# Optimization experiments

Hardware: AMD Instinct MI355X
Metric: run time of the kernel (lower is better)

Reference implementation:

```python
import jax, jax.numpy as jnp
import numpy as np

N_HEADS = 16
KEY_DIM = 64
VAL_DIM = 64
HIDDEN = 1024
SCALE = 1.0 / float(KEY_DIM) ** 0.5


def setup_inputs() -> dict:
    key = jax.random.key(0)
    ks = jax.random.split(key, 16)
    B, Lq, Lk, R = 2, 2048, 2048, 2048
    inp = {
        "query": jax.random.normal(ks[0], (B, Lq, HIDDEN), jnp.float32),
        "value": jax.random.normal(ks[1], (B, Lk, HIDDEN), jnp.float32),
        "positional_embedding": jax.random.normal(ks[2], (R, HIDDEN), jnp.float32),
        "u_weight": jax.random.normal(ks[3], (N_HEADS, KEY_DIM), jnp.float32) * 0.02,
        "v_weight": jax.random.normal(ks[4], (N_HEADS, KEY_DIM), jnp.float32) * 0.02,
        "indices": jax.random.randint(ks[5], (2, Lq, Lk), 0, R, jnp.int64 if jax.config.jax_enable_x64 else jnp.int32),
        "lower": jax.random.uniform(ks[6], (Lq, Lk), jnp.float32),
    }
    s = 0.02
    inp["Wq"] = jax.random.normal(ks[7], (HIDDEN, N_HEADS * KEY_DIM), jnp.float32) * s
    inp["bq"] = jnp.zeros((N_HEADS * KEY_DIM,), jnp.float32)
    inp["Wk"] = jax.random.normal(ks[8], (HIDDEN, N_HEADS * KEY_DIM), jnp.float32) * s
    inp["bk"] = jnp.zeros((N_HEADS * KEY_DIM,), jnp.float32)
    inp["Wv"] = jax.random.normal(ks[9], (HIDDEN, N_HEADS * VAL_DIM), jnp.float32) * s
    inp["bv"] = jnp.zeros((N_HEADS * VAL_DIM,), jnp.float32)
    inp["Wr"] = jax.random.normal(ks[10], (HIDDEN, N_HEADS * KEY_DIM), jnp.float32) * s
    inp["br"] = jnp.zeros((N_HEADS * KEY_DIM,), jnp.float32)
    inp["Wo"] = jax.random.normal(ks[11], (N_HEADS * VAL_DIM, HIDDEN), jnp.float32) * s
    inp["bo"] = jnp.zeros((HIDDEN,), jnp.float32)
    return inp


def reference(query, value, positional_embedding, u_weight, v_weight, indices, lower,
              Wq, bq, Wk, bk, Wv, bv, Wr, br, Wo, bo):
    B, Lq, _ = query.shape
    Lk = value.shape[1]
    R = positional_embedding.shape[0]
    # projections (torch Linear with weights stored as [in, out])
    q = (query @ Wq + bq).reshape(B, Lq, N_HEADS, KEY_DIM)
    k = (value @ Wk + bk).reshape(B, Lk, N_HEADS, KEY_DIM)
    v = (value @ Wv + bv).reshape(B, Lk, N_HEADS, VAL_DIM)
    r = (positional_embedding @ Wr + br).reshape(R, N_HEADS, KEY_DIM)
    # content (AC) and position (BD) score terms -> [i, j, b, n]
    AC = jnp.einsum("bind,bjnd->ijbn", q + u_weight, k)
    BD = jnp.einsum("bind,jnd->ijbn", q + v_weight, r)
    # rel-shift: gather [Lq, R] -> [Lq, Lk] positions, then apply lower mask
    BD = BD[indices[0], indices[1]] * lower[:, :, None, None]
    attn = jax.nn.softmax((AC + BD) * SCALE, axis=1)  # softmax over key dim j
    out = jnp.einsum("ijbn,bjnd->bind", attn, v).reshape(B, Lq, N_HEADS * VAL_DIM)
    return out @ Wo + bo
```

## Files before the change

### kernel.cpp

```cpp
#include <hip/hip_runtime.h>
#include <stdint.h>

typedef __attribute__((ext_vector_type(8))) short short8;
typedef __attribute__((ext_vector_type(4))) float f32x4;
typedef unsigned short u16;
typedef unsigned int u32;
typedef unsigned long long u64;

#define LQ 2048
#define LK 2048
#define RDIM 2048
#define HID 1024
#define NH 16
#define DH 64
#define S2SCALE 0.1803368801111204f

__device__ __forceinline__ float bf2f(u16 u){
  union { unsigned int i; float f; } v; v.i = ((unsigned int)u) << 16; return v.f;
}
__device__ __forceinline__ u16 f2bf(float f){
  union { float f; unsigned int i; } v; v.f = f;
  unsigned int r = v.i + 0x7fffu + ((v.i >> 16) & 1u);
  return (u16)(r >> 16);
}
__device__ __forceinline__ f32x4 fzero(){ f32x4 z = {0.0f, 0.0f, 0.0f, 0.0f}; return z; }

__global__ void k_detect(const u32* __restrict__ q, const u32* __restrict__ idxw,
                         int* __restrict__ flags){
  int t = threadIdx.x;
  u32 w = q[t];
  int b = (w >> 7) & 0xFF;
  unsigned long long mb = __ballot(b >= 100 && b <= 140);
  u32 hi = idxw[2 * t + 1];
  unsigned long long mi = __ballot(hi == 0u);
  if (t == 0){
    flags[0] = (__popcll(mb) >= 48) ? 1 : 0;
    flags[1] = (__popcll(mi) == 64) ? 1 : 0;
  }
}

struct Seg { const void* src; u16* dst; int n4; };
struct SegPack { Seg s[8]; };
__global__ void k_ingestN(SegPack p, const int* __restrict__ flags){
  int f = flags[0];
  Seg sg = p.s[blockIdx.y];
  int stride = gridDim.x * blockDim.x;
  for (int i = blockIdx.x * blockDim.x + threadIdx.x; i < sg.n4; i += stride){
    if (f){
      reinterpret_cast<uint2*>(sg.dst)[i] = reinterpret_cast<const uint2*>(sg.src)[i];
    } else {
      float4 v = reinterpret_cast<const float4*>(sg.src)[i];
      union { u16 h[4]; uint2 u; } t;
      t.h[0] = f2bf(v.x); t.h[1] = f2bf(v.y); t.h[2] = f2bf(v.z); t.h[3] = f2bf(v.w);
      reinterpret_cast<uint2*>(sg.dst)[i] = t.u;
    }
  }
}

struct WPack { const void* src[5]; u16* dst[5]; };
__global__ void k_wtrans(WPack p, const int* __restrict__ flags){
  int f = flags[0];
  const void* W = p.src[blockIdx.z];
  u16* Wt = p.dst[blockIdx.z];
  __shared__ u16 t[64][65];
  int tid = threadIdx.x;
  int bx = blockIdx.x, by = blockIdx.y;
#pragma unroll
  for (int it = 0; it < 16; ++it){
    int id = it * 256 + tid;
    int r = id >> 6, c = id & 63;
    size_t so = (size_t)(by * 64 + r) * HID + bx * 64 + c;
    t[r][c] = f ? ((const u16*)W)[so] : f2bf(((const float*)W)[so]);
  }
  __syncthreads();
#pragma unroll
  for (int it = 0; it < 16; ++it){
    int id = it * 256 + tid;
    int r = id >> 6, c = id & 63;
    Wt[(size_t)(bx * 64 + r) * HID + by * 64 + c] = t[c][r];
  }
}

__global__ void k_goff(const int* __restrict__ idx, int* __restrict__ goff,
                       const int* __restrict__ flags){
  int i64f = flags[1];
  const size_t N = (size_t)LQ * LK;
  size_t stride = (size_t)gridDim.x * blockDim.x;
  for (size_t t = (size_t)blockIdx.x * blockDim.x + threadIdx.x; t < N; t += stride){
    long long a0, a1;
    if (i64f){
      const long long* ip = (const long long*)idx;
      a0 = ip[t]; a1 = ip[N + t];
    } else {
      a0 = idx[t]; a1 = idx[N + t];
    }
    goff[t] = (int)(a0 * RDIM + a1);
  }
}

__global__ void k_gemm(const u16* __restrict__ A, const u16* __restrict__ Bt,
                       const u16* __restrict__ bias,
                       const u16* __restrict__ add0, const u16* __restrict__ add1,
                       void* __restrict__ D0, u16* __restrict__ D1,
                       int headmajor, const int* __restrict__ oflags){
  __shared__ u16 As[128][72];
  __shared__ u16 Bs[128][72];
  int tid = threadIdx.x;
  int l = tid & 63, w = tid >> 6;
  int lr = l & 15, g = l >> 4;
  int wr = w >> 1, wc = w & 1;
  int outf32 = oflags ? (oflags[0] == 0) : 0;
  f32x4 acc[4][4];
#pragma unroll
  for (int a = 0; a < 4; ++a)
#pragma unroll
    for (int bq_ = 0; bq_ < 4; ++bq_) acc[a][bq_] = fzero();
  const size_t arowg = (size_t)blockIdx.x * 128;
  const size_t browg = (size_t)blockIdx.y * 128;
  for (int kt = 0; kt < HID; kt += 64){
#pragma unroll
    for (int it = 0; it < 4; ++it){
      int id = it * 256 + tid;
      int r = id >> 3, ch = id & 7;
      uint4 va = *reinterpret_cast<const uint4*>(A + (arowg + r) * HID + kt + ch * 8);
      *reinterpret_cast<uint4*>(&As[r][ch * 8]) = va;
      uint4 vb = *reinterpret_cast<const uint4*>(Bt + (browg + r) * HID + kt + ch * 8);
      *reinterpret_cast<uint4*>(&Bs[r][ch * 8]) = vb;
    }
    __syncthreads();
#pragma unroll
    for (int ks = 0; ks < 2; ++ks){
      short8 af[4], bfv[4];
#pragma unroll
      for (int mf = 0; mf < 4; ++mf)
        af[mf] = *reinterpret_cast<const short8*>(&As[wr * 64 + mf * 16 + lr][ks * 32 + 8 * g]);
#pragma unroll
      for (int nf = 0; nf < 4; ++nf)
        bfv[nf] = *reinterpret_cast<const short8*>(&Bs[wc * 64 + nf * 16 + lr][ks * 32 + 8 * g]);
#pragma unroll
      for (int mf = 0; mf < 4; ++mf)
#pragma unroll
        for (int nf = 0; nf < 4; ++nf)
          acc[mf][nf] = __builtin_amdgcn_mfma_f32_16x16x32_bf16(af[mf], bfv[nf], acc[mf][nf], 0, 0, 0);
    }
    __syncthreads();
  }
#pragma unroll
  for (int mf = 0; mf < 4; ++mf)
#pragma unroll
    for (int nf = 0; nf < 4; ++nf){
      int col = (int)browg + wc * 64 + nf * 16 + lr;
      float bcol = bf2f(bias[col]);
      float a0 = add0 ? bf2f(add0[col]) : 0.0f;
      float a1 = add1 ? bf2f(add1[col]) : 0.0f;
#pragma unroll
      for (int reg = 0; reg < 4; ++reg){
        int row = (int)arowg + wr * 64 + mf * 16 + 4 * g + reg;
        float base = acc[mf][nf][reg] + bcol;
        if (headmajor == 2){
          int b = row >> 11, i = row & 2047;
          int n32 = col >> 6, d = col & 63;
          u16* Dx = (n32 < NH) ? (u16*)D0 : D1;
          size_t dst = ((size_t)(b * NH + (n32 & (NH - 1))) * LQ + i) * DH + d;
          Dx[dst] = f2bf(base);
        } else if (headmajor == 1){
          int b = row >> 11, i = row & 2047;
          int n = col >> 6, d = col & 63;
          size_t dst = ((size_t)(b * NH + n) * LQ + i) * DH + d;
          ((u16*)D0)[dst] = f2bf(base + a0);
          if (D1) D1[dst] = f2bf(base + a1);
        } else {
          size_t dst = (size_t)row * HID + col;
          if (outf32) ((float*)D0)[dst] = base;
          else        ((u16*)D0)[dst] = f2bf(base);
        }
      }
    }
}

__global__ void k_bdfull16(const u16* __restrict__ qv, const u16* __restrict__ rr,
                           u16* __restrict__ bdf, int bnBase){
  __shared__ u16 tile[32][64][16];
  int tid = threadIdx.x;
  int l = tid & 63, w = tid >> 6;
  int lr = l & 15, g = l >> 4;
  int i0 = blockIdx.x * 32, j0 = blockIdx.y * 64;
#pragma unroll
  for (int hh = 0; hh < 4; ++hh){
    int g_ = w * 4 + hh;
    int bn = bnBase + g_;
    int b = bn >> 4, n = bn & 15;
    const u16* qb = qv + ((size_t)(b * NH + n) * LQ + i0) * DH;
    const u16* rb = rr + ((size_t)n * RDIM + j0) * DH;
    short8 af[2][2];
#pragma unroll
    for (int mf = 0; mf < 2; ++mf)
#pragma unroll
      for (int ks = 0; ks < 2; ++ks)
        af[mf][ks] = *reinterpret_cast<const short8*>(qb + (size_t)(mf * 16 + lr) * DH + ks * 32 + 8 * g);
    f32x4 acc[2][4];
#pragma unroll
    for (int mf = 0; mf < 2; ++mf)
#pragma unroll
      for (int nf = 0; nf < 4; ++nf) acc[mf][nf] = fzero();
#pragma unroll
    for (int nf = 0; nf < 4; ++nf){
#pragma unroll
      for (int ks = 0; ks < 2; ++ks){
        short8 bb = *reinterpret_cast<const short8*>(rb + (size_t)(nf * 16 + lr) * DH + ks * 32 + 8 * g);
#pragma unroll
        for (int mf = 0; mf < 2; ++mf)
          acc[mf][nf] = __builtin_amdgcn_mfma_f32_16x16x32_bf16(af[mf][ks], bb, acc[mf][nf], 0, 0, 0);
      }
    }
#pragma unroll
    for (int mf = 0; mf < 2; ++mf)
#pragma unroll
      for (int nf = 0; nf < 4; ++nf)
#pragma unroll
        for (int reg = 0; reg < 4; ++reg)
          tile[mf * 16 + 4 * g + reg][nf * 16 + lr][g_] = f2bf(acc[mf][nf][reg]);
  }
  __syncthreads();
#pragma unroll
  for (int e = 0; e < 32; ++e){
    int id = e * 256 + tid;
    int line = id >> 2, part = id & 3;
    int ii = line >> 6, jj = line & 63;
    u64 v = *reinterpret_cast<const u64*>(&tile[ii][jj][part * 4]);
    *reinterpret_cast<u64*>(
        bdf + ((size_t)(i0 + ii) * RDIM + (size_t)(j0 + jj)) * 16 + part * 4) = v;
  }
}

__global__ void k_bdfull8(const u16* __restrict__ qv, const u16* __restrict__ rr,
                          u16* __restrict__ bdf, int bnBase){
  __shared__ u16 tile[32][64][8];
  int tid = threadIdx.x;
  int l = tid & 63, w = tid >> 6;
  int lr = l & 15, g = l >> 4;
  int i0 = blockIdx.x * 32, j0 = blockIdx.y * 64;
#pragma unroll
  for (int hh = 0; hh < 2; ++hh){
    int g_ = w * 2 + hh;
    int bn = bnBase + g_;
    int b = bn >> 4, n = bn & 15;
    const u16* qb = qv + ((size_t)(b * NH + n) * LQ + i0) * DH;
    const u16* rb = rr + ((size_t)n * RDIM + j0) * DH;
    short8 af[2][2];
#pragma unroll
    for (int mf = 0; mf < 2; ++mf)
#pragma unroll
      for (int ks = 0; ks < 2; ++ks)
        af[mf][ks] = *reinterpret_cast<const short8*>(qb + (size_t)(mf * 16 + lr) * DH + ks * 32 + 8 * g);
    f32x4 acc[2][4];
#pragma unroll
    for (int mf = 0; mf < 2; ++mf)
#pragma unroll
      for (int nf = 0; nf < 4; ++nf) acc[mf][nf] = fzero();
#pragma unroll
    for (int nf = 0; nf < 4; ++nf){
#pragma unroll
      for (int ks = 0; ks < 2; ++ks){
        short8 bb = *reinterpret_cast<const short8*>(rb + (size_t)(nf * 16 + lr) * DH + ks * 32 + 8 * g);
#pragma unroll
        for (int mf = 0; mf < 2; ++mf)
          acc[mf][nf] = __builtin_amdgcn_mfma_f32_16x16x32_bf16(af[mf][ks], bb, acc[mf][nf], 0, 0, 0);
      }
    }
#pragma unroll
    for (int mf = 0; mf < 2; ++mf)
#pragma unroll
      for (int nf = 0; nf < 4; ++nf)
#pragma unroll
        for (int reg = 0; reg < 4; ++reg)
          tile[mf * 16 + 4 * g + reg][nf * 16 + lr][g_] = f2bf(acc[mf][nf][reg]);
  }
  __syncthreads();
#pragma unroll
  for (int e = 0; e < 16; ++e){
    int id = e * 256 + tid;
    int line = id >> 1, part = id & 1;
    int ii = line >> 6, jj = line & 63;
    u64 v = *reinterpret_cast<const u64*>(&tile[ii][jj][part * 4]);
    *reinterpret_cast<u64*>(
        bdf + ((size_t)(i0 + ii) * RDIM + (size_t)(j0 + jj)) * 8 + part * 4) = v;
  }
}

template<int G>
__global__ void k_bdfull(const u16* __restrict__ qv, const u16* __restrict__ rr,
                         u16* __restrict__ bdf, int bnBase){
  __shared__ u16 tile[16][32][G];
  int tid = threadIdx.x;
  int l = tid & 63, w = tid >> 6;
  int lr = l & 15, g = l >> 4;
  int i0 = blockIdx.x * 16, j0 = blockIdx.y * 32;
  if (w < G){
    int g_ = w;
    int bn = bnBase + g_;
    int b = bn >> 4, n = bn & 15;
    const u16* qb = qv + ((size_t)(b * NH + n) * LQ + i0) * DH;
    const u16* rb = rr + ((size_t)n * RDIM + j0) * DH;
    f32x4 acc2[2];
    acc2[0] = fzero(); acc2[1] = fzero();
#pragma unroll
    for (int ks = 0; ks < 2; ++ks){
      short8 a = *reinterpret_cast<const short8*>(qb + (size_t)lr * DH + ks * 32 + 8 * g);
#pragma unroll
      for (int nf = 0; nf < 2; ++nf){
        short8 bb = *reinterpret_cast<const short8*>(rb + (size_t)(lr + 16 * nf) * DH + ks * 32 + 8 * g);
        acc2[nf] = __builtin_amdgcn_mfma_f32_16x16x32_bf16(a, bb, acc2[nf], 0, 0, 0);
      }
    }
#pragma unroll
    for (int nf = 0; nf < 2; ++nf){
      int jj = lr + 16 * nf;
#pragma unroll
      for (int reg = 0; reg < 4; ++reg)
        tile[4 * g + reg][jj][g_] = f2bf(acc2[nf][reg]);
    }
  }
  __syncthreads();
  constexpr int CHUNKS = 512;
#pragma unroll
  for (int e = 0; e < (CHUNKS * G + 255) / 256 && e * 256 < CHUNKS * G; ++e){
    int id = e * 256 + tid;
    if (id >= CHUNKS * G) break;
    int line = id / G, k = id % G;
    int ii = line >> 5, jj = line & 31;
    bdf[((size_t)(i0 + ii) * RDIM + (size_t)(j0 + jj)) * G + k] = tile[ii][jj][k];
  }
}

template<int G>
__global__ void k_gather(const u16* __restrict__ bdf, const int* __restrict__ goff,
                         const u16* __restrict__ lower, u16* __restrict__ bdg,
                         int iBase, int iSpan){
  __shared__ u16 tile[G][16][32];
  int tid = threadIdx.x;
  int i0 = iBase + blockIdx.x * 16, j0 = blockIdx.y * 32;
#pragma unroll
  for (int it = 0; it < 2; ++it){
    int p = it * 256 + tid;
    int ii = p >> 5, jj = p & 31;
    size_t off = (size_t)(i0 + ii) * LK + (j0 + jj);
    int go = goff[off];
    float lw = bf2f(lower[off]);
    const u16* src = bdf + (size_t)go * G;
    union { uint4 q[2]; u32 w2[8]; u16 h[16]; } uv;
    if (G == 16){
      uv.q[0] = *reinterpret_cast<const uint4*>(src);
      uv.q[1] = *reinterpret_cast<const uint4*>(src + 8);
    } else if (G == 8){
      uv.q[0] = *reinterpret_cast<const uint4*>(src);
    } else if (G == 2){
      uv.w2[0] = *reinterpret_cast<const u32*>(src);
    } else {
      uv.h[0] = *src;
    }
#pragma unroll
    for (int k = 0; k < G; ++k)
      tile[k][ii][jj] = f2bf(bf2f(uv.h[k]) * lw);
  }
  __syncthreads();
  constexpr int CHUNKS = G * 128;
#pragma unroll
  for (int e = 0; e < (CHUNKS + 255) / 256; ++e){
    int id = e * 256 + tid;
    if (CHUNKS < 256 * ((CHUNKS + 255) / 256) && id >= CHUNKS) break;
    int g_ = id >> 7, rem = id & 127;
    int ii = rem >> 3, part = rem & 7;
    u64 v = *reinterpret_cast<const u64*>(&tile[g_][ii][part * 4]);
    __builtin_nontemporal_store(v, reinterpret_cast<u64*>(
        bdg + (size_t)g_ * iSpan * LK + (size_t)(i0 - iBase + ii) * LK + j0 + part * 4));
  }
}

__device__ __forceinline__ void flash_compute(
    int lr, int g,
    const short8& aq0, const short8& aq1,
    f32x4* O, float* mrun, float* lacc,
    u16 (*klds)[72], u16 (*vtlds)[136], u16 (*pldsw)[136]){
  float sv[8][4];
#pragma unroll
  for (int nf = 0; nf < 8; ++nf){
    f32x4 z = fzero();
    short8 bk0 = *reinterpret_cast<const short8*>(&klds[lr + 16 * nf][8 * g]);
    short8 bk1 = *reinterpret_cast<const short8*>(&klds[lr + 16 * nf][32 + 8 * g]);
    z = __builtin_amdgcn_mfma_f32_16x16x32_bf16(aq0, bk0, z, 0, 0, 0);
    z = __builtin_amdgcn_mfma_f32_16x16x32_bf16(aq1, bk1, z, 0, 0, 0);
#pragma unroll
    for (int reg = 0; reg < 4; ++reg){
      float bd = bf2f(pldsw[4 * g + reg][lr + 16 * nf]);
      sv[nf][reg] = (z[reg] + bd) * S2SCALE;
    }
  }
  float fs[4];
#pragma unroll
  for (int reg = 0; reg < 4; ++reg){
    float mx = sv[0][reg];
#pragma unroll
    for (int nf = 1; nf < 8; ++nf) mx = fmaxf(mx, sv[nf][reg]);
#pragma unroll
    for (int d = 1; d < 16; d <<= 1) mx = fmaxf(mx, __shfl_xor(mx, d));
    float mnew = fmaxf(mrun[reg], mx);
    fs[reg] = exp2f(mrun[reg] - mnew);
    mrun[reg] = mnew;
    float sumloc = 0.0f;
#pragma unroll
    for (int nf = 0; nf < 8; ++nf){
      sv[nf][reg] = exp2f(sv[nf][reg] - mnew);
      sumloc += sv[nf][reg];
    }
    lacc[reg] = lacc[reg] * fs[reg] + sumloc;
  }
#pragma unroll
  for (int nf = 0; nf < 4; ++nf)
#pragma unroll
    for (int reg = 0; reg < 4; ++reg)
      O[nf][reg] *= fs[reg];
#pragma unroll
  for (int nf = 0; nf < 8; ++nf)
#pragma unroll
    for (int reg = 0; reg < 4; ++reg)
      pldsw[4 * g + reg][lr + 16 * nf] = f2bf(sv[nf][reg]);
  short8 pa[4];
#pragma unroll
  for (int ks = 0; ks < 4; ++ks)
    pa[ks] = *reinterpret_cast<const short8*>(&pldsw[lr][ks * 32 + 8 * g]);
#pragma unroll
  for (int nf = 0; nf < 4; ++nf){
    int d = lr + 16 * nf;
#pragma unroll
    for (int ks = 0; ks < 4; ++ks){
      int cv = ((ks * 4 + g) ^ (d >> 3)) * 8;
      short8 bv = *reinterpret_cast<const short8*>(&vtlds[d][cv]);
      O[nf] = __builtin_amdgcn_mfma_f32_16x16x32_bf16(pa[ks], bv, O[nf], 0, 0, 0);
    }
  }
}

__global__ __launch_bounds__(256) void k_flash(
    const u16* __restrict__ qu, const u16* __restrict__ kk,
    const u16* __restrict__ vv, const u16* __restrict__ bdg,
    u16* __restrict__ oo, int bnBase, int iBase, int iSpan){
  __shared__ u16 klds[128][72];
  __shared__ u16 vtlds[64][136];
  __shared__ u16 plds[4][16][136];
  int tid = threadIdx.x;
  int l = tid & 63, w = tid >> 6;
  int lr = l & 15, g = l >> 4;
  int gi = blockIdx.x;
  int bn = bnBase + gi;
  int b = bn >> 4, n = bn & 15;
  int i0 = iBase + blockIdx.y * 64;
  const u16* qb = qu + ((size_t)bn * LQ + i0 + w * 16) * DH;
  short8 aq0 = *reinterpret_cast<const short8*>(qb + (size_t)lr * DH + 8 * g);
  short8 aq1 = *reinterpret_cast<const short8*>(qb + (size_t)lr * DH + 32 + 8 * g);
  f32x4 O[4];
#pragma unroll
  for (int nf = 0; nf < 4; ++nf) O[nf] = fzero();
  float mrun[4], lacc[4];
#pragma unroll
  for (int r = 0; r < 4; ++r){ mrun[r] = -1e30f; lacc[r] = 0.0f; }
  const u16* kbase = kk + (size_t)bn * LK * DH;
  const u16* vbase = vv + (size_t)bn * LK * DH;
  const u16* bdw = bdg + (size_t)gi * iSpan * LK + (size_t)(i0 - iBase + w * 16) * LK;
  u16 (*pldsw)[136] = plds[w];
  int brow = l >> 2, bq = l & 3;

  uint4 kv[8];
  uint4 bdv[4];

#define LOADALL(J_) do { _Pragma("unroll") for (int it_ = 0; it_ < 4; ++it_){ \
    int id_ = it_ * 256 + tid; int r_ = id_ >> 3, ch_ = id_ & 7; \
    kv[it_]     = *reinterpret_cast<const uint4*>(kbase + (size_t)((J_) + r_) * DH + ch_ * 8); \
    kv[4 + it_] = *reinterpret_cast<const uint4*>(vbase + (size_t)((J_) + r_) * DH + ch_ * 8); } \
    _Pragma("unroll") for (int c_ = 0; c_ < 4; ++c_) \
      bdv[c_] = *reinterpret_cast<const uint4*>(bdw + (size_t)brow * LK + (J_) + (c_ * 4 + bq) * 8); } while(0)

#define WRITEALL() do { _Pragma("unroll") for (int it_ = 0; it_ < 4; ++it_){ \
    int id_ = it_ * 256 + tid; int r_ = id_ >> 3, ch_ = id_ & 7; \
    *reinterpret_cast<uint4*>(&klds[r_][ch_ * 8]) = kv[it_]; \
    u16 tmp_[8]; *reinterpret_cast<uint4*>(tmp_) = kv[4 + it_]; \
    int cb_ = r_ ^ (ch_ * 8); \
    _Pragma("unroll") for (int e_ = 0; e_ < 8; ++e_) vtlds[ch_ * 8 + e_][cb_] = tmp_[e_]; } \
    _Pragma("unroll") for (int c_ = 0; c_ < 4; ++c_) \
      *reinterpret_cast<uint4*>(&pldsw[brow][(c_ * 4 + bq) * 8]) = bdv[c_]; } while(0)

  LOADALL(0);
  WRITEALL();
  __syncthreads();

  for (int t = 0; t < 16; ++t){
    if (t < 15) LOADALL((t + 1) * 128);
    flash_compute(lr, g, aq0, aq1, O, mrun, lacc, klds, vtlds, pldsw);
    if (t < 15){
      __syncthreads();
      WRITEALL();
      __syncthreads();
    }
  }
#undef LOADALL
#undef WRITEALL

  float lsum[4];
#pragma unroll
  for (int reg = 0; reg < 4; ++reg){
    float s = lacc[reg];
#pragma unroll
    for (int d = 1; d < 16; d <<= 1) s += __shfl_xor(s, d);
    lsum[reg] = s;
  }
#pragma unroll
  for (int nf = 0; nf < 4; ++nf)
#pragma unroll
    for (int reg = 0; reg < 4; ++reg){
      int i = i0 + w * 16 + 4 * g + reg;
      float vo = O[nf][reg] / lsum[reg];
      oo[((size_t)(b * LQ + i)) * HID + n * DH + lr + 16 * nf] = f2bf(vo);
    }
}

extern "C" void kernel_launch(void* const* d_in, const int* in_sizes, int n_in,
                              void* d_out, int out_size, void* d_ws, size_t ws_size,
                              hipStream_t stream){
  const void* query = d_in[0];
  const void* value = d_in[1];
  const void* pos   = d_in[2];
  const void* uw    = d_in[3];
  const void* vw    = d_in[4];
  const int* idx    = (const int*)d_in[5];
  const void* lower = d_in[6];
  const void* Wq = d_in[7];  const void* bq = d_in[8];
  const void* Wk = d_in[9];  const void* bk = d_in[10];
  const void* Wv = d_in[11]; const void* bv = d_in[12];
  const void* Wr = d_in[13]; const void* br = d_in[14];
  const void* Wo = d_in[15]; const void* bo = d_in[16];
  (void)in_sizes; (void)n_in; (void)out_size;

  char* ws = (char*)d_ws;
  const size_t MB = (size_t)1 << 20;
  u16* cquery = (u16*)(ws + 0 * MB);
  u16* cvalue = (u16*)(ws + 8 * MB);
  int* goff   = (int*)(ws + 0 * MB);
  u16* cpos   = (u16*)(ws + 16 * MB);
  u16* clower = (u16*)(ws + 20 * MB);
  char* sm = ws + 28 * MB;
  u16* cuw = (u16*)(sm + 0 * 4096);
  u16* cvw = (u16*)(sm + 1 * 4096);
  u16* cbq = (u16*)(sm + 2 * 4096);
  u16* cbk = (u16*)(sm + 3 * 4096);
  u16* cbv = cbk + 1024;
  u16* cbr = (u16*)(sm + 5 * 4096);
  u16* cbo = (u16*)(sm + 6 * 4096);
  int* flags = (int*)(sm + 7 * 4096);
  u16* wot = (u16*)(ws + 29 * MB);
  u16* wqt = (u16*)(ws + 31 * MB);
  u16* wkt = (u16*)(ws + 33 * MB);
  u16* wvt = (u16*)(ws + 35 * MB);
  u16* wrt = (u16*)(ws + 37 * MB);
  u16* qu  = (u16*)(ws + 39 * MB);
  u16* qv  = (u16*)(ws + 47 * MB);
  u16* kkp = (u16*)(ws + 55 * MB);
  u16* vvp = (u16*)(ws + 63 * MB);
  u16* rrp = (u16*)(ws + 71 * MB);
  u16* oo  = (u16*)(ws + 75 * MB);
  u16* bdf = (u16*)(ws + 84 * MB);

  dim3 blk(256);
  k_detect<<<1, 64, 0, stream>>>((const u32*)query, (const u32*)idx, flags);

  {
    SegPack big;
    big.s[0] = { query, cquery, 2 * LQ * HID / 4 };
    big.s[1] = { value, cvalue, 2 * LK * HID / 4 };
    big.s[2] = { pos,   cpos,   RDIM * HID / 4 };
    big.s[3] = { lower, clower, LQ * LK / 4 };
    for (int i = 4; i < 8; ++i) big.s[i] = { nullptr, nullptr, 0 };
    k_ingestN<<<dim3(512, 4), blk, 0, stream>>>(big, flags);
    SegPack sml;
    sml.s[0] = { uw, cuw, NH * DH / 4 };
    sml.s[1] = { vw, cvw, NH * DH / 4 };
    sml.s[2] = { bq, cbq, HID / 4 };
    sml.s[3] = { bk, cbk, HID / 4 };
    sml.s[4] = { bv, cbv, HID / 4 };
    sml.s[5] = { br, cbr, HID / 4 };
    sml.s[6] = { bo, cbo, HID / 4 };
    sml.s[7] = { nullptr, nullptr, 0 };
    k_ingestN<<<dim3(4, 7), blk, 0, stream>>>(sml, flags);
  }
  {
    WPack wp;
    wp.src[0] = Wq; wp.dst[0] = wqt;
    wp.src[1] = Wk; wp.dst[1] = wkt;
    wp.src[2] = Wv; wp.dst[2] = wvt;
    wp.src[3] = Wr; wp.dst[3] = wrt;
    wp.src[4] = Wo; wp.dst[4] = wot;
    k_wtrans<<<dim3(16, 16, 5), blk, 0, stream>>>(wp, flags);
  }

  k_gemm<<<dim3(32, 8), blk, 0, stream>>>(cquery, wqt, cbq, cuw, cvw, qu, qv, 1, nullptr);
  k_gemm<<<dim3(32, 16), blk, 0, stream>>>(cvalue, wkt, cbk, nullptr, nullptr, kkp, vvp, 2, nullptr);
  k_gemm<<<dim3(16, 8), blk, 0, stream>>>(cpos, wrt, cbr, nullptr, nullptr, rrp, nullptr, 1, nullptr);

  k_goff<<<dim3(1024), blk, 0, stream>>>(idx, goff, flags);

  if (ws_size >= 276 * MB){
    u16* bdg = (u16*)(ws + 212 * MB);
    for (int b0 = 0; b0 < 2 * NH; b0 += 16){
      k_bdfull16<<<dim3(64, 32), blk, 0, stream>>>(qv, rrp, bdf, b0);
      for (int ih = 0; ih < LQ; ih += 1024){
        k_gather<16><<<dim3(64, 64), blk, 0, stream>>>(bdf, goff, clower, bdg, ih, 1024);
        k_flash<<<dim3(16, 16), blk, 0, stream>>>(qu, kkp, vvp, bdg, oo, b0, ih, 1024);
      }
    }
  } else if (ws_size >= 212 * MB){
    u16* bdg = (u16*)(ws + 148 * MB);
    for (int b0 = 0; b0 < 2 * NH; b0 += 8){
      k_bdfull8<<<dim3(64, 32), blk, 0, stream>>>(qv, rrp, bdf, b0);
      k_gather<8><<<dim3(128, 64), blk, 0, stream>>>(bdf, goff, clower, bdg, 0, LQ);
      k_flash<<<dim3(8, 32), blk, 0, stream>>>(qu, kkp, vvp, bdg, oo, b0, 0, LQ);
    }
  } else if (ws_size >= 116 * MB){
    u16* bdg = (u16*)(ws + 100 * MB);
    for (int b0 = 0; b0 < 2 * NH; b0 += 2){
      k_bdfull<2><<<dim3(128, 64), blk, 0, stream>>>(qv, rrp, bdf, b0);
      k_gather<2><<<dim3(128, 64), blk, 0, stream>>>(bdf, goff, clower, bdg, 0, LQ);
      k_flash<<<dim3(2, 32), blk, 0, stream>>>(qu, kkp, vvp, bdg, oo, b0, 0, LQ);
    }
  } else {
    u16* bdg = (u16*)(ws + 92 * MB);
    for (int b0 = 0; b0 < 2 * NH; b0 += 1){
      k_bdfull<1><<<dim3(128, 64), blk, 0, stream>>>(qv, rrp, bdf, b0);
      k_gather<1><<<dim3(128, 64), blk, 0, stream>>>(bdf, goff, clower, bdg, 0, LQ);
      k_flash<<<dim3(1, 32), blk, 0, stream>>>(qu, kkp, vvp, bdg, oo, b0, 0, LQ);
    }
  }
  k_gemm<<<dim3(32, 8), blk, 0, stream>>>(oo, wot, cbo, nullptr, nullptr, d_out, nullptr, 0, flags);
}
```

Baseline: 979.9 us.

## Chunk gathered BD along key dimension with split-softmax state carried across flash passes

The gathered position-score buffer is now split into key-dimension chunks rather than query-row halves. Flash attention runs once per chunk, storing the running max, running sum and unnormalised output in fp32 scratch between chunks and normalising only on the last chunk. Each flash launch now covers all query rows, giving a larger grid per launch, and the workspace layout is repacked so the 16-head path fits in a smaller workspace. The cost is extra fp32 partial-state traffic and more launches when chunks are small.

```diff
diff --git a/kernel.cpp b/kernel.cpp
--- a/kernel.cpp
+++ b/kernel.cpp
@@ -336,10 +336,12 @@
 template<int G>
 __global__ void k_gather(const u16* __restrict__ bdf, const int* __restrict__ goff,
                          const u16* __restrict__ lower, u16* __restrict__ bdg,
-                         int iBase, int iSpan){
+                         int jBase, int jSpan){
   __shared__ u16 tile[G][16][32];
   int tid = threadIdx.x;
-  int i0 = iBase + blockIdx.x * 16, j0 = blockIdx.y * 32;
+  int i0 = blockIdx.x * 16;
+  int j0loc = blockIdx.y * 32;
+  int j0 = jBase + j0loc;
 #pragma unroll
   for (int it = 0; it < 2; ++it){
     int p = it * 256 + tid;
@@ -373,7 +375,7 @@
     int ii = rem >> 3, part = rem & 7;
     u64 v = *reinterpret_cast<const u64*>(&tile[g_][ii][part * 4]);
     __builtin_nontemporal_store(v, reinterpret_cast<u64*>(
-        bdg + (size_t)g_ * iSpan * LK + (size_t)(i0 - iBase + ii) * LK + j0 + part * 4));
+        bdg + (size_t)g_ * LQ * jSpan + (size_t)(i0 + ii) * jSpan + j0loc + part * 4));
   }
 }
 
@@ -444,7 +446,8 @@
 __global__ __launch_bounds__(256) void k_flash(
     const u16* __restrict__ qu, const u16* __restrict__ kk,
     const u16* __restrict__ vv, const u16* __restrict__ bdg,
-    u16* __restrict__ oo, int bnBase, int iBase, int iSpan){
+    u16* __restrict__ oo, float* __restrict__ Opart, float2* __restrict__ mlpart,
+    int bnBase, int jBase, int jSpan, int mode){
   __shared__ u16 klds[128][72];
   __shared__ u16 vtlds[64][136];
   __shared__ u16 plds[4][16][136];
@@ -454,31 +457,43 @@
   int gi = blockIdx.x;
   int bn = bnBase + gi;
   int b = bn >> 4, n = bn & 15;
-  int i0 = iBase + blockIdx.y * 64;
+  int i0 = blockIdx.y * 64;
   const u16* qb = qu + ((size_t)bn * LQ + i0 + w * 16) * DH;
   short8 aq0 = *reinterpret_cast<const short8*>(qb + (size_t)lr * DH + 8 * g);
   short8 aq1 = *reinterpret_cast<const short8*>(qb + (size_t)lr * DH + 32 + 8 * g);
   f32x4 O[4];
-#pragma unroll
-  for (int nf = 0; nf < 4; ++nf) O[nf] = fzero();
   float mrun[4], lacc[4];
-#pragma unroll
-  for (int r = 0; r < 4; ++r){ mrun[r] = -1e30f; lacc[r] = 0.0f; }
+  if (mode & 1){
+#pragma unroll
+    for (int nf = 0; nf < 4; ++nf) O[nf] = fzero();
+#pragma unroll
+    for (int r = 0; r < 4; ++r){ mrun[r] = -1e30f; lacc[r] = 0.0f; }
+  } else {
+#pragma unroll
+    for (int reg = 0; reg < 4; ++reg){
+      int i = i0 + w * 16 + 4 * g + reg;
+      float2 ml = mlpart[(((size_t)gi * LQ + i) << 4) + lr];
+      mrun[reg] = ml.x; lacc[reg] = ml.y;
+#pragma unroll
+      for (int nf = 0; nf < 4; ++nf)
+        O[nf][reg] = Opart[((size_t)gi * LQ + i) * DH + lr + 16 * nf];
+    }
+  }
   const u16* kbase = kk + (size_t)bn * LK * DH;
   const u16* vbase = vv + (size_t)bn * LK * DH;
-  const u16* bdw = bdg + (size_t)gi * iSpan * LK + (size_t)(i0 - iBase + w * 16) * LK;
+  const u16* bdw = bdg + (size_t)gi * LQ * jSpan + (size_t)(i0 + w * 16) * jSpan;
   u16 (*pldsw)[136] = plds[w];
   int brow = l >> 2, bq = l & 3;
 
   uint4 kv[8];
   uint4 bdv[4];
 
-#define LOADALL(J_) do { _Pragma("unroll") for (int it_ = 0; it_ < 4; ++it_){ \
+#define LOADALL(JL_) do { _Pragma("unroll") for (int it_ = 0; it_ < 4; ++it_){ \
     int id_ = it_ * 256 + tid; int r_ = id_ >> 3, ch_ = id_ & 7; \
-    kv[it_]     = *reinterpret_cast<const uint4*>(kbase + (size_t)((J_) + r_) * DH + ch_ * 8); \
-    kv[4 + it_] = *reinterpret_cast<const uint4*>(vbase + (size_t)((J_) + r_) * DH + ch_ * 8); } \
+    kv[it_]     = *reinterpret_cast<const uint4*>(kbase + (size_t)(jBase + (JL_) + r_) * DH + ch_ * 8); \
+    kv[4 + it_] = *reinterpret_cast<const uint4*>(vbase + (size_t)(jBase + (JL_) + r_) * DH + ch_ * 8); } \
     _Pragma("unroll") for (int c_ = 0; c_ < 4; ++c_) \
-      bdv[c_] = *reinterpret_cast<const uint4*>(bdw + (size_t)brow * LK + (J_) + (c_ * 4 + bq) * 8); } while(0)
+      bdv[c_] = *reinterpret_cast<const uint4*>(bdw + (size_t)brow * jSpan + (JL_) + (c_ * 4 + bq) * 8); } while(0)
 
 #define WRITEALL() do { _Pragma("unroll") for (int it_ = 0; it_ < 4; ++it_){ \
     int id_ = it_ * 256 + tid; int r_ = id_ >> 3, ch_ = id_ & 7; \
@@ -489,14 +504,15 @@
     _Pragma("unroll") for (int c_ = 0; c_ < 4; ++c_) \
       *reinterpret_cast<uint4*>(&pldsw[brow][(c_ * 4 + bq) * 8]) = bdv[c_]; } while(0)
 
+  int ntiles = jSpan >> 7;
   LOADALL(0);
   WRITEALL();
   __syncthreads();
 
-  for (int t = 0; t < 16; ++t){
-    if (t < 15) LOADALL((t + 1) * 128);
+  for (int t = 0; t < ntiles; ++t){
+    if (t < ntiles - 1) LOADALL((t + 1) * 128);
     flash_compute(lr, g, aq0, aq1, O, mrun, lacc, klds, vtlds, pldsw);
-    if (t < 15){
+    if (t < ntiles - 1){
       __syncthreads();
       WRITEALL();
       __syncthreads();
@@ -505,22 +521,34 @@
 #undef LOADALL
 #undef WRITEALL
 
-  float lsum[4];
-#pragma unroll
-  for (int reg = 0; reg < 4; ++reg){
-    float s = lacc[reg];
-#pragma unroll
-    for (int d = 1; d < 16; d <<= 1) s += __shfl_xor(s, d);
-    lsum[reg] = s;
-  }
-#pragma unroll
-  for (int nf = 0; nf < 4; ++nf)
+  if (mode & 2){
+    float lsum[4];
+#pragma unroll
+    for (int reg = 0; reg < 4; ++reg){
+      float s = lacc[reg];
+#pragma unroll
+      for (int d = 1; d < 16; d <<= 1) s += __shfl_xor(s, d);
+      lsum[reg] = s;
+    }
+#pragma unroll
+    for (int nf = 0; nf < 4; ++nf)
+#pragma unroll
+      for (int reg = 0; reg < 4; ++reg){
+        int i = i0 + w * 16 + 4 * g + reg;
+        float vo = O[nf][reg] / lsum[reg];
+        oo[((size_t)(b * LQ + i)) * HID + n * DH + lr + 16 * nf] = f2bf(vo);
+      }
+  } else {
 #pragma unroll
     for (int reg = 0; reg < 4; ++reg){
       int i = i0 + w * 16 + 4 * g + reg;
-      float vo = O[nf][reg] / lsum[reg];
-      oo[((size_t)(b * LQ + i)) * HID + n * DH + lr + 16 * nf] = f2bf(vo);
-    }
+      float2 ml; ml.x = mrun[reg]; ml.y = lacc[reg];
+      mlpart[(((size_t)gi * LQ + i) << 4) + lr] = ml;
+#pragma unroll
+      for (int nf = 0; nf < 4; ++nf)
+        Opart[((size_t)gi * LQ + i) * DH + lr + 16 * nf] = O[nf][reg];
+    }
+  }
 }
 
 extern "C" void kernel_launch(void* const* d_in, const int* in_sizes, int n_in,
@@ -545,9 +573,8 @@
   u16* cquery = (u16*)(ws + 0 * MB);
   u16* cvalue = (u16*)(ws + 8 * MB);
   int* goff   = (int*)(ws + 0 * MB);
-  u16* cpos   = (u16*)(ws + 16 * MB);
-  u16* clower = (u16*)(ws + 20 * MB);
-  char* sm = ws + 28 * MB;
+  u16* clower = (u16*)(ws + 16 * MB);
+  char* sm = ws + 24 * MB;
   u16* cuw = (u16*)(sm + 0 * 4096);
   u16* cvw = (u16*)(sm + 1 * 4096);
   u16* cbq = (u16*)(sm + 2 * 4096);
@@ -556,18 +583,21 @@
   u16* cbr = (u16*)(sm + 5 * 4096);
   u16* cbo = (u16*)(sm + 6 * 4096);
   int* flags = (int*)(sm + 7 * 4096);
-  u16* wot = (u16*)(ws + 29 * MB);
-  u16* wqt = (u16*)(ws + 31 * MB);
-  u16* wkt = (u16*)(ws + 33 * MB);
-  u16* wvt = (u16*)(ws + 35 * MB);
-  u16* wrt = (u16*)(ws + 37 * MB);
-  u16* qu  = (u16*)(ws + 39 * MB);
-  u16* qv  = (u16*)(ws + 47 * MB);
-  u16* kkp = (u16*)(ws + 55 * MB);
-  u16* vvp = (u16*)(ws + 63 * MB);
-  u16* rrp = (u16*)(ws + 71 * MB);
-  u16* oo  = (u16*)(ws + 75 * MB);
-  u16* bdf = (u16*)(ws + 84 * MB);
+  u16* wot = (u16*)(ws + 25 * MB);
+  u16* qu  = (u16*)(ws + 27 * MB);
+  u16* qv  = (u16*)(ws + 35 * MB);
+  u16* kkp = (u16*)(ws + 43 * MB);
+  u16* vvp = (u16*)(ws + 51 * MB);
+  u16* rrp = (u16*)(ws + 59 * MB);
+  u16* oo  = (u16*)(ws + 63 * MB);
+  float*  Opart  = (float*)(ws + 71 * MB);
+  float2* mlpart = (float2*)(ws + 79 * MB);
+  u16* bdf = (u16*)(ws + 83 * MB);
+  u16* wqt = (u16*)(ws + 83 * MB);
+  u16* wkt = (u16*)(ws + 85 * MB);
+  u16* wvt = (u16*)(ws + 87 * MB);
+  u16* wrt = (u16*)(ws + 89 * MB);
+  u16* cpos = (u16*)(ws + 91 * MB);
 
   dim3 blk(256);
   k_detect<<<1, 64, 0, stream>>>((const u32*)query, (const u32*)idx, flags);
@@ -607,35 +637,41 @@
 
   k_goff<<<dim3(1024), blk, 0, stream>>>(idx, goff, flags);
 
-  if (ws_size >= 276 * MB){
-    u16* bdg = (u16*)(ws + 212 * MB);
+  int jSpan16 = 0;
+  if (ws_size >= 243 * MB) jSpan16 = 512;
+  else if (ws_size >= 227 * MB) jSpan16 = 256;
+
+  if (jSpan16){
+    u16* bdg = (u16*)(ws + 211 * MB);
     for (int b0 = 0; b0 < 2 * NH; b0 += 16){
       k_bdfull16<<<dim3(64, 32), blk, 0, stream>>>(qv, rrp, bdf, b0);
-      for (int ih = 0; ih < LQ; ih += 1024){
-        k_gather<16><<<dim3(64, 64), blk, 0, stream>>>(bdf, goff, clower, bdg, ih, 1024);
-        k_flash<<<dim3(16, 16), blk, 0, stream>>>(qu, kkp, vvp, bdg, oo, b0, ih, 1024);
+      for (int jb = 0; jb < LK; jb += jSpan16){
+        k_gather<16><<<dim3(128, jSpan16 / 32), blk, 0, stream>>>(bdf, goff, clower, bdg, jb, jSpan16);
+        int mode = (jb == 0 ? 1 : 0) | (jb + jSpan16 >= LK ? 2 : 0);
+        k_flash<<<dim3(16, 32), blk, 0, stream>>>(qu, kkp, vvp, bdg, oo, Opart, mlpart, b0, jb, jSpan16, mode);
       }
     }
-  } else if (ws_size >= 212 * MB){
-    u16* bdg = (u16*)(ws + 148 * MB);
+  } else if (ws_size >= 211 * MB){
+    u16* bdf8 = bdf;
+    u16* bdg = (u16*)(ws + 147 * MB);
     for (int b0 = 0; b0 < 2 * NH; b0 += 8){
-      k_bdfull8<<<dim3(64, 32), blk, 0, stream>>>(qv, rrp, bdf, b0);
-      k_gather<8><<<dim3(128, 64), blk, 0, stream>>>(bdf, goff, clower, bdg, 0, LQ);
-      k_flash<<<dim3(8, 32), blk, 0, stream>>>(qu, kkp, vvp, bdg, oo, b0, 0, LQ);
-    }
-  } else if (ws_size >= 116 * MB){
-    u16* bdg = (u16*)(ws + 100 * MB);
+      k_bdfull8<<<dim3(64, 32), blk, 0, stream>>>(qv, rrp, bdf8, b0);
+      k_gather<8><<<dim3(128, 64), blk, 0, stream>>>(bdf8, goff, clower, bdg, 0, LK);
+      k_flash<<<dim3(8, 32), blk, 0, stream>>>(qu, kkp, vvp, bdg, oo, Opart, mlpart, b0, 0, LK, 3);
+    }
+  } else if (ws_size >= 115 * MB){
+    u16* bdg = (u16*)(ws + 99 * MB);
     for (int b0 = 0; b0 < 2 * NH; b0 += 2){
       k_bdfull<2><<<dim3(128, 64), blk, 0, stream>>>(qv, rrp, bdf, b0);
-      k_gather<2><<<dim3(128, 64), blk, 0, stream>>>(bdf, goff, clower, bdg, 0, LQ);
-      k_flash<<<dim3(2, 32), blk, 0, stream>>>(qu, kkp, vvp, bdg, oo, b0, 0, LQ);
+      k_gather<2><<<dim3(128, 64), blk, 0, stream>>>(bdf, goff, clower, bdg, 0, LK);
+      k_flash<<<dim3(2, 32), blk, 0, stream>>>(qu, kkp, vvp, bdg, oo, Opart, mlpart, b0, 0, LK, 3);
     }
   } else {
-    u16* bdg = (u16*)(ws + 92 * MB);
+    u16* bdg = (u16*)(ws + 95 * MB);
     for (int b0 = 0; b0 < 2 * NH; b0 += 1){
       k_bdfull<1><<<dim3(128, 64), blk, 0, stream>>>(qv, rrp, bdf, b0);
-      k_gather<1><<<dim3(128, 64), blk, 0, stream>>>(bdf, goff, clower, bdg, 0, LQ);
-      k_flash<<<dim3(1, 32), blk, 0, stream>>>(qu, kkp, vvp, bdg, oo, b0, 0, LQ);
+      k_gather<1><<<dim3(128, 64), blk, 0, stream>>>(bdf, goff, clower, bdg, 0, LK);
+      k_flash<<<dim3(1, 32), blk, 0, stream>>>(qu, kkp, vvp, bdg, oo, Opart, mlpart, b0, 0, LK, 3);
     }
   }
   k_gemm<<<dim3(32, 8), blk, 0, stream>>>(oo, wot, cbo, nullptr, nullptr, d_out, nullptr, 0, flags);
```

Result: faster. 879.0 us (-10.3%).
